# Kernel tuning notes

Measured on AMD Instinct MI355X. Metric: run time of the kernel, lower is better.

Reference implementation:

```python
import jax, jax.numpy as jnp
import numpy as np
from jax import lax

V, E, H = 32000, 256, 512
B, S_SRC, S_TGT = 32, 128, 64


def setup_inputs() -> dict:
    key = jax.random.key(0)
    ks = jax.random.split(key, 16)
    n = lambda k, shp: jax.random.normal(k, shp, dtype=jnp.float32) * 0.05
    return {
        "src": jax.random.randint(ks[0], (B, S_SRC), 0, V, dtype=jnp.int32),
        "tgt": jax.random.randint(ks[1], (B, S_TGT), 0, V, dtype=jnp.int32),
        "enc_emb": n(ks[2], (V, E)),
        "enc_Wih": n(ks[3], (4 * H, E)),
        "enc_Whh": n(ks[4], (4 * H, H)),
        "enc_b": n(ks[5], (4 * H,)),
        "attn_W": n(ks[6], (H, 2 * H)),
        "attn_b": n(ks[7], (H,)),
        "attn_v": jax.random.uniform(ks[8], (H,), dtype=jnp.float32),
        "dec_emb": n(ks[9], (V, E)),
        "dec_Wih": n(ks[10], (4 * H, E + H)),
        "dec_Whh": n(ks[11], (4 * H, H)),
        "dec_b": n(ks[12], (4 * H,)),
        "out_W": n(ks[13], (V, H)),
        "out_b": n(ks[14], (V,)),
    }


def _lstm_cell(x, h, c, Wih, Whh, b):
    # PyTorch gate order: i, f, g, o. b = b_ih + b_hh fused.
    z = x @ Wih.T + h @ Whh.T + b  # [B, 4H]
    i, f, g, o = jnp.split(z, 4, axis=-1)
    c_new = jax.nn.sigmoid(f) * c + jax.nn.sigmoid(i) * jnp.tanh(g)
    h_new = jax.nn.sigmoid(o) * jnp.tanh(c_new)
    return h_new, c_new


def reference(src, tgt, enc_emb, enc_Wih, enc_Whh, enc_b, attn_W, attn_b,
              attn_v, dec_emb, dec_Wih, dec_Whh, dec_b, out_W, out_b):
    b = src.shape[0]
    h0 = jnp.zeros((b, H), dtype=enc_emb.dtype)
    c0 = jnp.zeros((b, H), dtype=enc_emb.dtype)

    # ---- Encoder: single-layer LSTM over src ----
    emb_src = enc_emb[src]  # [B, S_src, E]

    def enc_step(carry, x_t):
        h, c = carry
        h, c = _lstm_cell(x_t, h, c, enc_Wih, enc_Whh, enc_b)
        return (h, c), h

    (h, c), enc_out = lax.scan(enc_step, (h0, c0), emb_src.transpose(1, 0, 2))
    enc_out = enc_out.transpose(1, 0, 2)  # [B, S_src, H]

    # attn_W acts on cat([hidden, enc]); split into hidden and encoder parts.
    W_h = attn_W[:, :H]   # [H, H]
    W_e = attn_W[:, H:]   # [H, H]
    enc_proj = jnp.einsum('bsh,kh->bsk', enc_out, W_e)  # precomputed [B, S, H]

    # ---- Decoder with per-step Bahdanau attention ----
    emb_tgt = dec_emb[tgt].transpose(1, 0, 2)  # [T, B, E]

    def dec_step(carry, e_t):
        h, c = carry
        energy = jnp.tanh(enc_proj + (h @ W_h.T + attn_b)[:, None, :])  # [B,S,H]
        score = energy @ attn_v                                          # [B,S]
        a = jax.nn.softmax(score, axis=1)
        context = jnp.einsum('bs,bsh->bh', a, enc_out)                   # [B,H]
        x = jnp.concatenate([e_t, context], axis=-1)                     # [B,E+H]
        h, c = _lstm_cell(x, h, c, dec_Wih, dec_Whh, dec_b)
        return (h, c), h

    _, dec_h = lax.scan(dec_step, (h, c), emb_tgt)
    dec_h = dec_h.transpose(1, 0, 2)  # [B, T, H]

    return dec_h @ out_W.T + out_b  # [B, T, V]
```

## Files before the change

kernel.cpp:

```cpp
#include <hip/hip_runtime.h>

#define B_    32
#define SSRC  128
#define STGT  64
#define E_    256
#define H_    512
#define G4    2048
#define V_    32000

typedef unsigned short u16;
typedef short bf16x8 __attribute__((ext_vector_type(8)));
typedef float f32x4 __attribute__((ext_vector_type(4)));

__device__ __forceinline__ u16 f2b(float f) {
  unsigned u = __float_as_uint(f);
  u += 0x7FFFu + ((u >> 16) & 1u);
  return (u16)(u >> 16);
}
__device__ __forceinline__ float b2f(u16 h) {
  return __uint_as_float(((unsigned)h) << 16);
}
__device__ __forceinline__ unsigned pk2(float lo, float hi) {
  return (unsigned)f2b(lo) | (((unsigned)f2b(hi)) << 16);
}
__device__ __forceinline__ float sigm(float x) { return 1.0f / (1.0f + __expf(-x)); }
__device__ __forceinline__ float tanh_(float x) { return 1.0f - 2.0f / (1.0f + __expf(2.0f * x)); }

#if defined(__has_builtin)
#if __has_builtin(__builtin_amdgcn_fdot2_f32_bf16)
#define HAS_DOT2 1
#endif
#endif
#ifdef HAS_DOT2
typedef __bf16 b162 __attribute__((ext_vector_type(2)));
__device__ __forceinline__ float dot2u(unsigned a, unsigned b, float acc) {
  return __builtin_amdgcn_fdot2_f32_bf16(__builtin_bit_cast(b162, a),
                                         __builtin_bit_cast(b162, b), acc, false);
}
#else
__device__ __forceinline__ float dot2u(unsigned a, unsigned b, float acc) {
  acc += __uint_as_float(a << 16) * __uint_as_float(b << 16);
  acc += __uint_as_float(a & 0xffff0000u) * __uint_as_float(b & 0xffff0000u);
  return acc;
}
#endif
__device__ __forceinline__ float dot4(uint4 w, uint4 h, float acc) {
  return dot2u(w.w, h.w, dot2u(w.z, h.z, dot2u(w.y, h.y, dot2u(w.x, h.x, acc))));
}

__device__ __forceinline__ int swz64(int c) {
  return (c & ~3) | ((c & 3) ^ ((c >> 3) & 3));
}

__device__ __forceinline__ uint4 cload4(const void* p) {
  uint4 r;
  asm volatile("global_load_dwordx4 %0, %1, off sc0 sc1\n\ts_waitcnt vmcnt(0)"
               : "=&v"(r) : "v"(p) : "memory");
  return r;
}
__device__ __forceinline__ void cload4x2(uint4& a, uint4& b, const void* pa, const void* pb) {
  asm volatile("global_load_dwordx4 %0, %2, off sc0 sc1\n\t"
               "global_load_dwordx4 %1, %3, off sc0 sc1\n\t"
               "s_waitcnt vmcnt(0)"
               : "=&v"(a), "=&v"(b) : "v"(pa), "v"(pb) : "memory");
}
__device__ __forceinline__ void cstoreu(unsigned* p, unsigned v) {
  asm volatile("global_store_dword %0, %1, off sc0 sc1" :: "v"(p), "v"(v) : "memory");
}
__device__ __forceinline__ void cstore4(unsigned* p, uint4 v) {
  cstoreu(p + 0, v.x);
  cstoreu(p + 1, v.y);
  cstoreu(p + 2, v.z);
  cstoreu(p + 3, v.w);
}

__device__ __forceinline__ void gbar(int* flags, int myid, int target) {
  asm volatile("s_waitcnt vmcnt(0)" ::: "memory");
  __syncthreads();
  if (threadIdx.x == 0)
    __hip_atomic_store(flags + myid, target, __ATOMIC_RELAXED, __HIP_MEMORY_SCOPE_AGENT);
  if (threadIdx.x < 64) {
    int l = threadIdx.x & 31;
    while (__hip_atomic_load(flags + l, __ATOMIC_RELAXED, __HIP_MEMORY_SCOPE_AGENT) < target)
      __builtin_amdgcn_s_sleep(1);
  }
  __syncthreads();
  asm volatile("" ::: "memory");
}

__global__ void prep_kernel(const int* __restrict__ src, const int* __restrict__ tgt,
                            const float* __restrict__ enc_emb, const float* __restrict__ dec_emb,
                            const float* __restrict__ enc_Wih, const float* __restrict__ dec_Wih,
                            const float* __restrict__ attn_W, const float* __restrict__ out_W,
                            u16* __restrict__ A_enc, u16* __restrict__ A_dec,
                            u16* __restrict__ WihE, u16* __restrict__ WihD,
                            u16* __restrict__ Web, u16* __restrict__ WihCp,
                            u16* __restrict__ outWb)
{
  const long n_outw = (long)V_ * H_;
  const long n_aenc = (long)B_ * SSRC * E_;
  const long n_adec = (long)B_ * STGT * E_;
  const long n_wih  = (long)G4 * E_;
  const long n_web  = (long)H_ * H_;
  const long n_wcp  = (long)G4 * H_;
  const long total = n_outw + n_aenc + n_adec + 2 * n_wih + n_web + n_wcp;
  for (long i = (long)blockIdx.x * blockDim.x + threadIdx.x; i < total;
       i += (long)gridDim.x * blockDim.x) {
    long x = i;
    if (x < n_outw) { outWb[x] = f2b(out_W[x]); continue; }
    x -= n_outw;
    if (x < n_aenc) {
      int row = (int)(x >> 8), e = (int)(x & 255);
      A_enc[x] = f2b(enc_emb[(size_t)src[row] * E_ + e]);
      continue;
    }
    x -= n_aenc;
    if (x < n_adec) {
      int row = (int)(x >> 8), e = (int)(x & 255);
      A_dec[x] = f2b(dec_emb[(size_t)tgt[row] * E_ + e]);
      continue;
    }
    x -= n_adec;
    if (x < n_wih) { WihE[x] = f2b(enc_Wih[x]); continue; }
    x -= n_wih;
    if (x < n_wih) {
      int r = (int)(x >> 8), e = (int)(x & 255);
      WihD[x] = f2b(dec_Wih[(size_t)r * 768 + e]);
      continue;
    }
    x -= n_wih;
    if (x < n_web) {
      int d = (int)(x >> 9), k = (int)(x & 511);
      Web[x] = f2b(attn_W[(size_t)d * 1024 + 512 + k]);
      continue;
    }
    x -= n_web;
    {
      int n = (int)(x >> 9), k = (int)(x & 511);
      int gb = n >> 6, gate = (n >> 4) & 3, jl = n & 15;
      int orig = gate * 512 + gb * 16 + jl;
      WihCp[x] = f2b(dec_Wih[(size_t)orig * 768 + 256 + k]);
    }
  }
}

template<int KTOT, bool OBF>
__global__ __launch_bounds__(256, 2) void gemm_nt(
    const u16* __restrict__ A, const u16* __restrict__ Bm,
    const float* __restrict__ bias, void* __restrict__ Cv, int M, int N)
{
  int nbm = M >> 7;
  int bn = blockIdx.x / nbm;
  int bm = blockIdx.x % nbm;
  int w = threadIdx.x >> 6, l = threadIdx.x & 63;
  int wr = w >> 1, wc = w & 1;
  int m0 = bm * 128 + wr * 64, n0 = bn * 128 + wc * 64;
  int lr = l & 15, ko = (l >> 4) * 8;
  f32x4 acc[4][4] = {};
  const u16* Ap = A + (size_t)(m0 + lr) * KTOT + ko;
  const u16* Bp = Bm + (size_t)(n0 + lr) * KTOT + ko;
  for (int k0 = 0; k0 < KTOT; k0 += 32) {
    bf16x8 af[4], bfr[4];
#pragma unroll
    for (int i = 0; i < 4; ++i) af[i] = *(const bf16x8*)(Ap + (size_t)i * 16 * KTOT + k0);
#pragma unroll
    for (int i = 0; i < 4; ++i) bfr[i] = *(const bf16x8*)(Bp + (size_t)i * 16 * KTOT + k0);
#pragma unroll
    for (int i = 0; i < 4; ++i)
#pragma unroll
      for (int j = 0; j < 4; ++j)
        acc[i][j] = __builtin_amdgcn_mfma_f32_16x16x32_bf16(af[i], bfr[j], acc[i][j], 0, 0, 0);
  }
  int rbase = (l >> 4) * 4;
#pragma unroll
  for (int i = 0; i < 4; ++i) {
#pragma unroll
    for (int j = 0; j < 4; ++j) {
      int gn = n0 + j * 16 + lr;
      float bv = bias ? bias[gn] : 0.f;
#pragma unroll
      for (int r = 0; r < 4; ++r) {
        int gm = m0 + i * 16 + rbase + r;
        float v = acc[i][j][r] + bv;
        if (OBF) ((u16*)Cv)[(size_t)gm * N + gn] = f2b(v);
        else     ((float*)Cv)[(size_t)gm * N + gn] = v;
      }
    }
  }
}

__device__ __forceinline__ void zgemv64(int tid, const uint4* Wu, const uint4* Hu,
                                        float (*part)[64][4]) {
  int rq = tid >> 4, kq = tid & 15;
  float acc[4][4] = {};
#pragma unroll
  for (int u = 0; u < 4; ++u) {
    int sc = swz64(kq * 4 + u);
    uint4 h0 = Hu[sc], h1 = Hu[64 + sc], h2 = Hu[128 + sc], h3 = Hu[192 + sc];
#pragma unroll
    for (int r = 0; r < 4; ++r) {
      uint4 wv = Wu[(rq * 4 + r) * 64 + sc];
      acc[r][0] = dot4(wv, h0, acc[r][0]);
      acc[r][1] = dot4(wv, h1, acc[r][1]);
      acc[r][2] = dot4(wv, h2, acc[r][2]);
      acc[r][3] = dot4(wv, h3, acc[r][3]);
    }
  }
#pragma unroll
  for (int r = 0; r < 4; ++r) {
    float4 v = {acc[r][0], acc[r][1], acc[r][2], acc[r][3]};
    *(float4*)&part[kq][(rq * 4 + r) ^ (kq & 7)][0] = v;
  }
}

template<typename GrowF>
__device__ __forceinline__ void fillw64(int tid, const float* Wsrc, uint4* Wu, GrowF grow) {
#pragma unroll 4
  for (int i = 0; i < 16; ++i) {
    int idx4 = tid + i * 256;
    int row = idx4 >> 6, c = idx4 & 63;
    const float* s = Wsrc + (size_t)grow(row) * 512 + c * 8;
    float4 a = *(const float4*)s, b4 = *(const float4*)(s + 4);
    uint4 pkv = {pk2(a.x, a.y), pk2(a.z, a.w), pk2(b4.x, b4.y), pk2(b4.z, b4.w)};
    Wu[row * 64 + swz64(c)] = pkv;
  }
}

__global__ __launch_bounds__(256, 1) void encoder_kernel(
    const float* __restrict__ enc_Whh, const u16* __restrict__ encXW,
    unsigned* __restrict__ h16buf ,
    float* __restrict__ cfin, u16* __restrict__ eo_g, int* __restrict__ bars)
{
  const int tid = threadIdx.x;
  const int g = blockIdx.x & 7;
  const int gb = blockIdx.x >> 3;
  const int b0 = g * 4;
  const int ds0 = gb * 16;
  int* flags = bars + g * 64;
  int ep_ = 0;

  __shared__ uint4 encW4[64 * 64];
  __shared__ uint4 hl16[4 * 64];
  __shared__ float part[16][64][4];
  __shared__ float zx[4][64];
  __shared__ float cS[4][16];

  if (tid < 64) cS[tid >> 4][tid & 15] = 0.f;
  fillw64(tid, enc_Whh, encW4, [&](int row) { return (row >> 4) * 512 + ds0 + (row & 15); });
  __syncthreads();

  for (int t = 0; t < SSRC; ++t) {
    {
      int row = tid >> 6, c = tid & 63;
      uint4 v = cload4((const uint4*)h16buf + (size_t)(t & 1) * 2048 + (b0 + row) * 64 + c);
      hl16[row * 64 + swz64(c)] = v;
    }
    __syncthreads();
    zgemv64(tid, encW4, hl16, part);
    __syncthreads();
    {
      int b_l = tid >> 6, rl = tid & 63;
      float z = 0.f;
#pragma unroll
      for (int kq = 0; kq < 16; ++kq) z += part[kq][rl ^ (kq & 7)][b_l];
      int grow = (rl >> 4) * 512 + ds0 + (rl & 15);
      z += b2f(encXW[((size_t)(b0 + b_l) * SSRC + t) * G4 + grow]);
      zx[b_l][rl] = z;
    }
    __syncthreads();
    if (tid < 64) {
      int bl = tid >> 4, jl = tid & 15;
      float iv = zx[bl][jl], fv = zx[bl][16 + jl], gv = zx[bl][32 + jl], ov = zx[bl][48 + jl];
      float cn = sigm(fv) * cS[bl][jl] + sigm(iv) * tanh_(gv);
      float hn = sigm(ov) * tanh_(cn);
      cS[bl][jl] = cn;
      eo_g[((size_t)(b0 + bl) * SSRC + t) * H_ + ds0 + jl] = f2b(hn);
      float hn1 = __shfl_down(hn, 1);
      if ((jl & 1) == 0)
        cstoreu(h16buf + (size_t)((t + 1) & 1) * 8192 + (size_t)(b0 + bl) * 256 + gb * 8 + (jl >> 1),
                pk2(hn, hn1));
    }
    gbar(flags, gb, ++ep_);
  }
  if (tid < 64)
    cfin[(size_t)(b0 + (tid >> 4)) * H_ + ds0 + (tid & 15)] = cS[tid >> 4][tid & 15];
}

__global__ __launch_bounds__(256, 1) void decoder_kernel(
    const float* __restrict__ dec_Whh, const float* __restrict__ attn_W,
    const float* __restrict__ attn_b, const float* __restrict__ attn_v,
    const u16* __restrict__ eprojb, const u16* __restrict__ decXW,
    const u16* __restrict__ eoPb,
    unsigned* __restrict__ hd16 , const float* __restrict__ cfin,
    float* __restrict__ qg , float* __restrict__ scoreb ,
    u16* __restrict__ dech, int* __restrict__ bars)
{
  const int tid = threadIdx.x;
  const int g = blockIdx.x & 7;
  const int gb = blockIdx.x >> 3;
  const int b0 = g * 4;
  const int ds0 = gb * 16;
  int* flags = bars + g * 64;
  int ep_ = 0;

  __shared__ uint4 decW4[64 * 64];
  __shared__ uint4 Whb4[16 * 64];
  __shared__ uint4 hl16[4 * 64];
  __shared__ float part[16][64][4];
  __shared__ float partE[8][64][4];
  __shared__ float4 qf4[4 * 128];
  __shared__ float4 vf4[128];
  __shared__ float scoreS[4][128];
  __shared__ float aS[4][128];
  __shared__ float zx[4][64];
  __shared__ __align__(16) float qS[4][16];
  __shared__ __align__(16) float scr16[4][4];
  __shared__ float cS[4][16];
  __shared__ float bS[16];

  if (tid < 64) cS[tid >> 4][tid & 15] = cfin[(size_t)(b0 + (tid >> 4)) * H_ + ds0 + (tid & 15)];
  if (tid < 16) bS[tid] = attn_b[ds0 + tid];
  if (tid < 128) {
    float4 v = *(const float4*)(attn_v + tid * 4);
    vf4[tid ^ ((tid >> 3) & 7)] = v;
  }
  fillw64(tid, dec_Whh, decW4, [&](int row) { return (row >> 4) * 512 + ds0 + (row & 15); });
#pragma unroll
  for (int i = 0; i < 4; ++i) {
    int idx4 = tid + i * 256;
    int row = idx4 >> 6, c = idx4 & 63;
    const float* s = attn_W + (size_t)(ds0 + row) * 1024 + c * 8;
    float4 a = *(const float4*)s, b4 = *(const float4*)(s + 4);
    uint4 pkv = {pk2(a.x, a.y), pk2(a.z, a.w), pk2(b4.x, b4.y), pk2(b4.z, b4.w)};
    Whb4[row * 64 + (c ^ (row & 7))] = pkv;
  }
  __syncthreads();

  for (int t = 0; t < STGT; ++t) {
    {
      int row = tid >> 6, c = tid & 63;
      uint4 v = cload4((const uint4*)hd16 + (b0 + row) * 64 + c);
      hl16[row * 64 + swz64(c)] = v;
    }
    __syncthreads();
    {
      int b_l = tid >> 6, d_l = (tid >> 2) & 15, kq4 = tid & 3;
      float acc = 0.f;
#pragma unroll
      for (int u = 0; u < 16; ++u) {
        int c = kq4 * 16 + u;
        uint4 wv = Whb4[d_l * 64 + (c ^ (d_l & 7))];
        uint4 hv = hl16[b_l * 64 + swz64(c)];
        acc = dot4(wv, hv, acc);
      }
      acc += __shfl_xor(acc, 1);
      acc += __shfl_xor(acc, 2);
      if (kq4 == 0) qS[b_l][d_l] = acc + bS[d_l];
    }
    __syncthreads();
    if (tid < 16) {
      float4 v = *(float4*)&qS[tid >> 2][(tid & 3) * 4];
      cstore4((unsigned*)(qg + (size_t)(g * 4 + (tid >> 2)) * 512 + ds0 + (tid & 3) * 4),
              *(uint4*)&v);
    }
    gbar(flags, gb, ++ep_);

    {
      int b_l = tid >> 6, c = tid & 63;
      uint4 a, b4;
      const float* sp = qg + (size_t)(g * 4 + b_l) * 512 + c * 8;
      cload4x2(a, b4, sp, sp + 4);
      int lw0 = c * 2, lw1 = c * 2 + 1;
      qf4[b_l * 128 + (lw0 ^ ((lw0 >> 3) & 7))] = *(float4*)&a;
      qf4[b_l * 128 + (lw1 ^ ((lw1 >> 3) & 7))] = *(float4*)&b4;
    }
    __syncthreads();
    {
      int p = tid >> 4, lane16 = tid & 15;
      int b_l = p >> 2, s_l = p & 3;
      int s = gb * 4 + s_l;
      const uint4* ep = (const uint4*)(eprojb + ((size_t)(b0 + b_l) * SSRC + s) * H_) + lane16 * 4;
      uint4 e0 = ep[0], e1 = ep[1], e2 = ep[2], e3 = ep[3];
      unsigned ev[8] = {e0.x, e0.y, e0.z, e0.w, e1.x, e1.y, e1.z, e1.w};
      unsigned ev2[8] = {e2.x, e2.y, e2.z, e2.w, e3.x, e3.y, e3.z, e3.w};
      float acc = 0.f;
#pragma unroll
      for (int i = 0; i < 8; ++i) {
        int lr = lane16 * 8 + i;
        float4 q = qf4[b_l * 128 + (lr ^ ((lr >> 3) & 7))];
        float4 vv = vf4[lr ^ ((lr >> 3) & 7)];
        unsigned lo = (i < 4) ? ev[i * 2] : ev2[(i - 4) * 2];
        unsigned hi = (i < 4) ? ev[i * 2 + 1] : ev2[(i - 4) * 2 + 1];
        acc += vv.x * tanh_(b2f((u16)(lo & 0xffff)) + q.x);
        acc += vv.y * tanh_(b2f((u16)(lo >> 16)) + q.y);
        acc += vv.z * tanh_(b2f((u16)(hi & 0xffff)) + q.z);
        acc += vv.w * tanh_(b2f((u16)(hi >> 16)) + q.w);
      }
      acc += __shfl_xor(acc, 1);
      acc += __shfl_xor(acc, 2);
      acc += __shfl_xor(acc, 4);
      acc += __shfl_xor(acc, 8);
      if (lane16 == 0) scr16[b_l][s_l] = acc;
    }
    __syncthreads();
    if (tid < 4) {
      float4 v = *(float4*)&scr16[tid][0];
      cstore4((unsigned*)(scoreb + (size_t)(g * 4 + tid) * 128 + gb * 4), *(uint4*)&v);
    }
    gbar(flags, gb, ++ep_);

    if (tid < 128) {
      int row = tid >> 5, c4 = tid & 31;
      uint4 vv = cload4(scoreb + (size_t)(g * 4 + row) * 128 + c4 * 4);
      *(float4*)&scoreS[row][c4 * 4] = *(float4*)&vv;
    }
    zgemv64(tid, decW4, hl16, part);
    __syncthreads();
    {
      int w = tid >> 6, lane = tid & 63;
      float s1 = scoreS[w][lane], s2v = scoreS[w][64 + lane];
      float m = fmaxf(s1, s2v);
#pragma unroll
      for (int off = 32; off; off >>= 1) m = fmaxf(m, __shfl_xor(m, off));
      float e1 = __expf(s1 - m), e2 = __expf(s2v - m);
      float sm = e1 + e2;
#pragma unroll
      for (int off = 32; off; off >>= 1) sm += __shfl_xor(sm, off);
      float inv = 1.0f / sm;
      aS[w][lane] = e1 * inv;
      aS[w][64 + lane] = e2 * inv;
    }
    __syncthreads();
    {
      int sq = tid >> 5, cp = tid & 31;
      const unsigned* eoPu = (const unsigned*)eoPb;
      float a0 = 0.f, a1 = 0.f, a2 = 0.f, a3 = 0.f, a4 = 0.f, a5 = 0.f, a6 = 0.f, a7 = 0.f;
#pragma unroll 4
      for (int s = sq * 16; s < sq * 16 + 16; ++s) {
        unsigned u0 = eoPu[((size_t)(b0 + 0) * SSRC + s) * 1024 + gb * 32 + cp];
        unsigned u1 = eoPu[((size_t)(b0 + 1) * SSRC + s) * 1024 + gb * 32 + cp];
        unsigned u2 = eoPu[((size_t)(b0 + 2) * SSRC + s) * 1024 + gb * 32 + cp];
        unsigned u3 = eoPu[((size_t)(b0 + 3) * SSRC + s) * 1024 + gb * 32 + cp];
        float w0 = aS[0][s], w1 = aS[1][s], w2 = aS[2][s], w3 = aS[3][s];
        a0 += w0 * b2f((u16)(u0 & 0xffff)); a1 += w0 * b2f((u16)(u0 >> 16));
        a2 += w1 * b2f((u16)(u1 & 0xffff)); a3 += w1 * b2f((u16)(u1 >> 16));
        a4 += w2 * b2f((u16)(u2 & 0xffff)); a5 += w2 * b2f((u16)(u2 >> 16));
        a6 += w3 * b2f((u16)(u3 & 0xffff)); a7 += w3 * b2f((u16)(u3 >> 16));
      }
      float4 lo = {a0, a2, a4, a6}, hi = {a1, a3, a5, a7};
      *(float4*)&partE[sq][cp * 2][0] = lo;
      *(float4*)&partE[sq][cp * 2 + 1][0] = hi;
    }
    __syncthreads();
    {
      int b_l = tid >> 6, rl = tid & 63;
      float z = 0.f;
#pragma unroll
      for (int kq = 0; kq < 16; ++kq) z += part[kq][rl ^ (kq & 7)][b_l];
#pragma unroll
      for (int sq = 0; sq < 8; ++sq) z += partE[sq][rl][b_l];
      int grow = (rl >> 4) * 512 + ds0 + (rl & 15);
      z += b2f(decXW[((size_t)(b0 + b_l) * STGT + t) * G4 + grow]);
      zx[b_l][rl] = z;
    }
    __syncthreads();
    if (tid < 64) {
      int bl = tid >> 4, jl = tid & 15;
      float iv = zx[bl][jl], fv = zx[bl][16 + jl], gv = zx[bl][32 + jl], ov = zx[bl][48 + jl];
      float cn = sigm(fv) * cS[bl][jl] + sigm(iv) * tanh_(gv);
      float hn = sigm(ov) * tanh_(cn);
      cS[bl][jl] = cn;
      dech[((size_t)(b0 + bl) * STGT + t) * H_ + ds0 + jl] = f2b(hn);
      float hn1 = __shfl_down(hn, 1);
      if ((jl & 1) == 0)
        cstoreu(hd16 + (size_t)(b0 + bl) * 256 + gb * 8 + (jl >> 1), pk2(hn, hn1));
    }
    gbar(flags, gb, ++ep_);
  }
}

#define OFF_BARE   0u
#define OFF_BARD   2048u
#define OFF_H16    4096u
#define OFF_CFIN   69632u
#define OFF_QG     135168u
#define OFF_SCORE  200704u
#define OFF_AENC   262144u
#define OFF_ADEC   2359296u
#define OFF_WIHE   3407872u
#define OFF_WIHD   4456448u
#define OFF_WEB    5505024u
#define OFF_WIHCP  6029312u
#define OFF_OUTW   8126464u
#define OFF_ENCXW  40894464u
#define OFF_DECXW  57671680u
#define OFF_EO     66060288u
#define OFF_EPROJ  70254592u
#define OFF_DECH   74448896u

extern "C" void kernel_launch(void* const* d_in, const int* in_sizes, int n_in,
                              void* d_out, int out_size, void* d_ws, size_t ws_size,
                              hipStream_t stream)
{
  const int*   src     = (const int*)d_in[0];
  const int*   tgt     = (const int*)d_in[1];
  const float* enc_emb = (const float*)d_in[2];
  const float* enc_Wih = (const float*)d_in[3];
  const float* enc_Whh = (const float*)d_in[4];
  const float* enc_b   = (const float*)d_in[5];
  const float* attn_W  = (const float*)d_in[6];
  const float* attn_b  = (const float*)d_in[7];
  const float* attn_v  = (const float*)d_in[8];
  const float* dec_emb = (const float*)d_in[9];
  const float* dec_Wih = (const float*)d_in[10];
  const float* dec_Whh = (const float*)d_in[11];
  const float* dec_b   = (const float*)d_in[12];
  const float* out_W   = (const float*)d_in[13];
  const float* out_b   = (const float*)d_in[14];

  char* ws = (char*)d_ws;
  int*      barE   = (int*)(ws + OFF_BARE);
  int*      barD   = (int*)(ws + OFF_BARD);
  unsigned* h16buf = (unsigned*)(ws + OFF_H16);
  float*    cfin   = (float*)(ws + OFF_CFIN);
  float*    qg     = (float*)(ws + OFF_QG);
  float*    scoreb = (float*)(ws + OFF_SCORE);
  u16*      A_enc  = (u16*)(ws + OFF_AENC);
  u16*      A_dec  = (u16*)(ws + OFF_ADEC);
  u16*      WihE   = (u16*)(ws + OFF_WIHE);
  u16*      WihD   = (u16*)(ws + OFF_WIHD);
  u16*      Web    = (u16*)(ws + OFF_WEB);
  u16*      WihCp  = (u16*)(ws + OFF_WIHCP);
  u16*      outWb  = (u16*)(ws + OFF_OUTW);
  u16*      encXW  = (u16*)(ws + OFF_ENCXW);
  u16*      eoPb   = (u16*)(ws + OFF_ENCXW);
  u16*      decXW  = (u16*)(ws + OFF_DECXW);
  u16*      eo_g   = (u16*)(ws + OFF_EO);
  u16*      eprojb = (u16*)(ws + OFF_EPROJ);
  u16*      dech   = (u16*)(ws + OFF_DECH);

  (void)hipMemsetAsync(d_ws, 0, OFF_H16 + 65536, stream);

  prep_kernel<<<2048, 256, 0, stream>>>(src, tgt, enc_emb, dec_emb, enc_Wih, dec_Wih,
                                        attn_W, out_W, A_enc, A_dec, WihE, WihD, Web, WihCp, outWb);

  gemm_nt<256, true><<<512, 256, 0, stream>>>(A_enc, WihE, enc_b, (void*)encXW, 4096, 2048);
  gemm_nt<256, true><<<256, 256, 0, stream>>>(A_dec, WihD, dec_b, (void*)decXW, 2048, 2048);

  encoder_kernel<<<256, 256, 0, stream>>>(enc_Whh, encXW, h16buf, cfin, eo_g, barE);

  gemm_nt<512, true><<<128, 256, 0, stream>>>(eo_g, Web, nullptr, (void*)eprojb, 4096, 512);
  gemm_nt<512, true><<<512, 256, 0, stream>>>(eo_g, WihCp, nullptr, (void*)eoPb, 4096, 2048);

  decoder_kernel<<<256, 256, 0, stream>>>(dec_Whh, attn_W, attn_b, attn_v,
                                          eprojb, decXW, eoPb, h16buf, cfin,
                                          qg, scoreb, dech, barD);

  gemm_nt<512, false><<<4000, 256, 0, stream>>>(dech, outWb, out_b, d_out, 2048, 32000);
}
```

Baseline: 1.555 ms.

## Fuse encoder projections into recurrent loop and cut decoder attention barriers

The encoder kernel now computes the attention encoder projection and the context-times-Wih projection for the previous step's hidden state inside its barrier wait window, which removes two separate GEMM launches and the eo_g intermediate. The decoder replaces the global query exchange plus score exchange (two barriers) with per-block partial scores over each block's own 16 hidden dimensions, written to a buffer and reduced after a single split arrive/wait barrier that overlaps the Whh GEMV. Encoder-output projections are also preloaded into registers once per block. The cost is extra serial work per encoder step, many small scattered global stores, and a 32-way cross-block reduction of partial scores on every decoder step.

```diff
diff --git a/kernel.cpp b/kernel.cpp
--- a/kernel.cpp
+++ b/kernel.cpp
@@ -9,6 +9,7 @@
 #define V_    32000
 
 typedef unsigned short u16;
+typedef unsigned long long u64b;
 typedef short bf16x8 __attribute__((ext_vector_type(8)));
 typedef float f32x4 __attribute__((ext_vector_type(4)));
 
@@ -58,27 +59,23 @@
                : "=&v"(r) : "v"(p) : "memory");
   return r;
 }
-__device__ __forceinline__ void cload4x2(uint4& a, uint4& b, const void* pa, const void* pb) {
-  asm volatile("global_load_dwordx4 %0, %2, off sc0 sc1\n\t"
-               "global_load_dwordx4 %1, %3, off sc0 sc1\n\t"
-               "s_waitcnt vmcnt(0)"
-               : "=&v"(a), "=&v"(b) : "v"(pa), "v"(pb) : "memory");
+__device__ __forceinline__ void cstoref(float* p, float v) {
+  asm volatile("global_store_dword %0, %1, off sc0 sc1" :: "v"(p), "v"(v) : "memory");
 }
 __device__ __forceinline__ void cstoreu(unsigned* p, unsigned v) {
   asm volatile("global_store_dword %0, %1, off sc0 sc1" :: "v"(p), "v"(v) : "memory");
 }
-__device__ __forceinline__ void cstore4(unsigned* p, uint4 v) {
-  cstoreu(p + 0, v.x);
-  cstoreu(p + 1, v.y);
-  cstoreu(p + 2, v.z);
-  cstoreu(p + 3, v.w);
-}
-
-__device__ __forceinline__ void gbar(int* flags, int myid, int target) {
+__device__ __forceinline__ float cloadf_relaxed(const float* p) {
+  return __hip_atomic_load(p, __ATOMIC_RELAXED, __HIP_MEMORY_SCOPE_AGENT);
+}
+
+__device__ __forceinline__ void arrive(int* flags, int myid, int target) {
   asm volatile("s_waitcnt vmcnt(0)" ::: "memory");
   __syncthreads();
   if (threadIdx.x == 0)
     __hip_atomic_store(flags + myid, target, __ATOMIC_RELAXED, __HIP_MEMORY_SCOPE_AGENT);
+}
+__device__ __forceinline__ void waitbar(int* flags, int target) {
   if (threadIdx.x < 64) {
     int l = threadIdx.x & 31;
     while (__hip_atomic_load(flags + l, __ATOMIC_RELAXED, __HIP_MEMORY_SCOPE_AGENT) < target)
@@ -91,19 +88,17 @@
 __global__ void prep_kernel(const int* __restrict__ src, const int* __restrict__ tgt,
                             const float* __restrict__ enc_emb, const float* __restrict__ dec_emb,
                             const float* __restrict__ enc_Wih, const float* __restrict__ dec_Wih,
-                            const float* __restrict__ attn_W, const float* __restrict__ out_W,
+                            const float* __restrict__ out_W,
                             u16* __restrict__ A_enc, u16* __restrict__ A_dec,
                             u16* __restrict__ WihE, u16* __restrict__ WihD,
-                            u16* __restrict__ Web, u16* __restrict__ WihCp,
-                            u16* __restrict__ outWb)
+                            u16* __restrict__ WihC, u16* __restrict__ outWb)
 {
   const long n_outw = (long)V_ * H_;
   const long n_aenc = (long)B_ * SSRC * E_;
   const long n_adec = (long)B_ * STGT * E_;
   const long n_wih  = (long)G4 * E_;
-  const long n_web  = (long)H_ * H_;
   const long n_wcp  = (long)G4 * H_;
-  const long total = n_outw + n_aenc + n_adec + 2 * n_wih + n_web + n_wcp;
+  const long total = n_outw + n_aenc + n_adec + 2 * n_wih + n_wcp;
   for (long i = (long)blockIdx.x * blockDim.x + threadIdx.x; i < total;
        i += (long)gridDim.x * blockDim.x) {
     long x = i;
@@ -129,17 +124,9 @@
       continue;
     }
     x -= n_wih;
-    if (x < n_web) {
-      int d = (int)(x >> 9), k = (int)(x & 511);
-      Web[x] = f2b(attn_W[(size_t)d * 1024 + 512 + k]);
-      continue;
-    }
-    x -= n_web;
-    {
-      int n = (int)(x >> 9), k = (int)(x & 511);
-      int gb = n >> 6, gate = (n >> 4) & 3, jl = n & 15;
-      int orig = gate * 512 + gb * 16 + jl;
-      WihCp[x] = f2b(dec_Wih[(size_t)orig * 768 + 256 + k]);
+    {
+      int r = (int)(x >> 9), k = (int)(x & 511);
+      WihC[x] = f2b(dec_Wih[(size_t)r * 768 + 256 + k]);
     }
   }
 }
@@ -177,7 +164,7 @@
 #pragma unroll
     for (int j = 0; j < 4; ++j) {
       int gn = n0 + j * 16 + lr;
-      float bv = bias ? bias[gn] : 0.f;
+      float bv = bias[gn];
 #pragma unroll
       for (int r = 0; r < 4; ++r) {
         int gm = m0 + i * 16 + rbase + r;
@@ -227,9 +214,10 @@
 }
 
 __global__ __launch_bounds__(256, 1) void encoder_kernel(
-    const float* __restrict__ enc_Whh, const u16* __restrict__ encXW,
-    unsigned* __restrict__ h16buf ,
-    float* __restrict__ cfin, u16* __restrict__ eo_g, int* __restrict__ bars)
+    const float* __restrict__ enc_Whh, const float* __restrict__ attn_W,
+    const u16* __restrict__ WihC, const u16* __restrict__ encXW,
+    unsigned* __restrict__ h16buf, float* __restrict__ cfin,
+    u16* __restrict__ eprojb, u16* __restrict__ eoPw, int* __restrict__ bars)
 {
   const int tid = threadIdx.x;
   const int g = blockIdx.x & 7;
@@ -237,9 +225,9 @@
   const int b0 = g * 4;
   const int ds0 = gb * 16;
   int* flags = bars + g * 64;
-  int ep_ = 0;
 
   __shared__ uint4 encW4[64 * 64];
+  __shared__ uint4 web4[16 * 64];
   __shared__ uint4 hl16[4 * 64];
   __shared__ float part[16][64][4];
   __shared__ float zx[4][64];
@@ -247,6 +235,15 @@
 
   if (tid < 64) cS[tid >> 4][tid & 15] = 0.f;
   fillw64(tid, enc_Whh, encW4, [&](int row) { return (row >> 4) * 512 + ds0 + (row & 15); });
+#pragma unroll
+  for (int i = 0; i < 4; ++i) {
+    int idx4 = tid + i * 256;
+    int row = idx4 >> 6, c = idx4 & 63;
+    const float* s = attn_W + (size_t)(ds0 + row) * 1024 + 512 + c * 8;
+    float4 a = *(const float4*)s, b4 = *(const float4*)(s + 4);
+    uint4 pkv = {pk2(a.x, a.y), pk2(a.z, a.w), pk2(b4.x, b4.y), pk2(b4.z, b4.w)};
+    web4[row * 64 + (c ^ (row & 7))] = pkv;
+  }
   __syncthreads();
 
   for (int t = 0; t < SSRC; ++t) {
@@ -274,13 +271,103 @@
       float cn = sigm(fv) * cS[bl][jl] + sigm(iv) * tanh_(gv);
       float hn = sigm(ov) * tanh_(cn);
       cS[bl][jl] = cn;
-      eo_g[((size_t)(b0 + bl) * SSRC + t) * H_ + ds0 + jl] = f2b(hn);
       float hn1 = __shfl_down(hn, 1);
       if ((jl & 1) == 0)
         cstoreu(h16buf + (size_t)((t + 1) & 1) * 8192 + (size_t)(b0 + bl) * 256 + gb * 8 + (jl >> 1),
                 pk2(hn, hn1));
     }
-    gbar(flags, gb, ++ep_);
+    arrive(flags, gb, t + 1);
+    if (t > 0) {
+      int tm1 = t - 1;
+      {
+        int d_l = tid >> 4, b_l = (tid >> 2) & 3, kq4 = tid & 3;
+        float acc = 0.f;
+#pragma unroll
+        for (int u = 0; u < 16; ++u) {
+          int c = kq4 * 16 + u;
+          acc = dot4(web4[d_l * 64 + (c ^ (d_l & 7))], hl16[b_l * 64 + swz64(c)], acc);
+        }
+        acc += __shfl_xor(acc, 1);
+        acc += __shfl_xor(acc, 2);
+        if (kq4 == 0)
+          eprojb[(((size_t)(b0 + b_l) * SSRC + tm1) << 9) + ds0 + d_l] = f2b(acc);
+      }
+      {
+        int r = tid >> 2, kq4 = tid & 3;
+        int n = (r >> 4) * 512 + ds0 + (r & 15);
+        const uint4* wr_ = (const uint4*)(WihC + (size_t)n * 512) + kq4 * 16;
+        float a0 = 0.f, a1 = 0.f, a2 = 0.f, a3 = 0.f;
+#pragma unroll
+        for (int u = 0; u < 16; ++u) {
+          uint4 wv = wr_[u];
+          int sc = swz64(kq4 * 16 + u);
+          a0 = dot4(wv, hl16[sc], a0);
+          a1 = dot4(wv, hl16[64 + sc], a1);
+          a2 = dot4(wv, hl16[128 + sc], a2);
+          a3 = dot4(wv, hl16[192 + sc], a3);
+        }
+        a0 += __shfl_xor(a0, 1); a0 += __shfl_xor(a0, 2);
+        a1 += __shfl_xor(a1, 1); a1 += __shfl_xor(a1, 2);
+        a2 += __shfl_xor(a2, 1); a2 += __shfl_xor(a2, 2);
+        a3 += __shfl_xor(a3, 1); a3 += __shfl_xor(a3, 2);
+        if (kq4 == 0) {
+          size_t base = ((size_t)b0 * SSRC + tm1) << 11;
+          eoPw[base + n] = f2b(a0);
+          eoPw[base + (SSRC << 11) + n] = f2b(a1);
+          eoPw[base + (2u * SSRC << 11) + n] = f2b(a2);
+          eoPw[base + (3u * SSRC << 11) + n] = f2b(a3);
+        }
+      }
+    }
+    waitbar(flags, t + 1);
+  }
+  {
+    int row = tid >> 6, c = tid & 63;
+    uint4 v = cload4((const uint4*)h16buf + (b0 + row) * 64 + c);
+    hl16[row * 64 + swz64(c)] = v;
+  }
+  __syncthreads();
+  {
+    int tm1 = SSRC - 1;
+    {
+      int d_l = tid >> 4, b_l = (tid >> 2) & 3, kq4 = tid & 3;
+      float acc = 0.f;
+#pragma unroll
+      for (int u = 0; u < 16; ++u) {
+        int c = kq4 * 16 + u;
+        acc = dot4(web4[d_l * 64 + (c ^ (d_l & 7))], hl16[b_l * 64 + swz64(c)], acc);
+      }
+      acc += __shfl_xor(acc, 1);
+      acc += __shfl_xor(acc, 2);
+      if (kq4 == 0)
+        eprojb[(((size_t)(b0 + b_l) * SSRC + tm1) << 9) + ds0 + d_l] = f2b(acc);
+    }
+    {
+      int r = tid >> 2, kq4 = tid & 3;
+      int n = (r >> 4) * 512 + ds0 + (r & 15);
+      const uint4* wr_ = (const uint4*)(WihC + (size_t)n * 512) + kq4 * 16;
+      float a0 = 0.f, a1 = 0.f, a2 = 0.f, a3 = 0.f;
+#pragma unroll
+      for (int u = 0; u < 16; ++u) {
+        uint4 wv = wr_[u];
+        int sc = swz64(kq4 * 16 + u);
+        a0 = dot4(wv, hl16[sc], a0);
+        a1 = dot4(wv, hl16[64 + sc], a1);
+        a2 = dot4(wv, hl16[128 + sc], a2);
+        a3 = dot4(wv, hl16[192 + sc], a3);
+      }
+      a0 += __shfl_xor(a0, 1); a0 += __shfl_xor(a0, 2);
+      a1 += __shfl_xor(a1, 1); a1 += __shfl_xor(a1, 2);
+      a2 += __shfl_xor(a2, 1); a2 += __shfl_xor(a2, 2);
+      a3 += __shfl_xor(a3, 1); a3 += __shfl_xor(a3, 2);
+      if (kq4 == 0) {
+        size_t base = ((size_t)b0 * SSRC + tm1) << 11;
+        eoPw[base + n] = f2b(a0);
+        eoPw[base + (SSRC << 11) + n] = f2b(a1);
+        eoPw[base + (2u * SSRC << 11) + n] = f2b(a2);
+        eoPw[base + (3u * SSRC << 11) + n] = f2b(a3);
+      }
+    }
   }
   if (tid < 64)
     cfin[(size_t)(b0 + (tid >> 4)) * H_ + ds0 + (tid & 15)] = cS[tid >> 4][tid & 15];
@@ -291,8 +378,8 @@
     const float* __restrict__ attn_b, const float* __restrict__ attn_v,
     const u16* __restrict__ eprojb, const u16* __restrict__ decXW,
     const u16* __restrict__ eoPb,
-    unsigned* __restrict__ hd16 , const float* __restrict__ cfin,
-    float* __restrict__ qg , float* __restrict__ scoreb ,
+    unsigned* __restrict__ hd16, const float* __restrict__ cfin,
+    float* __restrict__ vpart ,
     u16* __restrict__ dech, int* __restrict__ bars)
 {
   const int tid = threadIdx.x;
@@ -308,22 +395,15 @@
   __shared__ uint4 hl16[4 * 64];
   __shared__ float part[16][64][4];
   __shared__ float partE[8][64][4];
-  __shared__ float4 qf4[4 * 128];
-  __shared__ float4 vf4[128];
   __shared__ float scoreS[4][128];
   __shared__ float aS[4][128];
   __shared__ float zx[4][64];
-  __shared__ __align__(16) float qS[4][16];
-  __shared__ __align__(16) float scr16[4][4];
+  __shared__ float qS[4][16];
   __shared__ float cS[4][16];
-  __shared__ float bS[16];
+  __shared__ float vS[16], bS[16];
 
   if (tid < 64) cS[tid >> 4][tid & 15] = cfin[(size_t)(b0 + (tid >> 4)) * H_ + ds0 + (tid & 15)];
-  if (tid < 16) bS[tid] = attn_b[ds0 + tid];
-  if (tid < 128) {
-    float4 v = *(const float4*)(attn_v + tid * 4);
-    vf4[tid ^ ((tid >> 3) & 7)] = v;
-  }
+  if (tid < 16) { vS[tid] = attn_v[ds0 + tid]; bS[tid] = attn_b[ds0 + tid]; }
   fillw64(tid, dec_Whh, decW4, [&](int row) { return (row >> 4) * 512 + ds0 + (row & 15); });
 #pragma unroll
   for (int i = 0; i < 4; ++i) {
@@ -334,6 +414,20 @@
     uint4 pkv = {pk2(a.x, a.y), pk2(a.z, a.w), pk2(b4.x, b4.y), pk2(b4.z, b4.w)};
     Whb4[row * 64 + (c ^ (row & 7))] = pkv;
   }
+  const int sq = tid >> 5, cp = tid & 31;
+  const int n32 = (cp >> 3) * 256 + gb * 8 + (cp & 7);
+  uint4 eor[16];
+  {
+    const unsigned* eoPu = (const unsigned*)eoPb;
+#pragma unroll
+    for (int si = 0; si < 16; ++si) {
+      int s = sq * 16 + si;
+      eor[si].x = eoPu[((size_t)(b0 + 0) * SSRC + s) * 1024 + n32];
+      eor[si].y = eoPu[((size_t)(b0 + 1) * SSRC + s) * 1024 + n32];
+      eor[si].z = eoPu[((size_t)(b0 + 2) * SSRC + s) * 1024 + n32];
+      eor[si].w = eoPu[((size_t)(b0 + 3) * SSRC + s) * 1024 + n32];
+    }
+  }
   __syncthreads();
 
   for (int t = 0; t < STGT; ++t) {
@@ -349,72 +443,57 @@
 #pragma unroll
       for (int u = 0; u < 16; ++u) {
         int c = kq4 * 16 + u;
-        uint4 wv = Whb4[d_l * 64 + (c ^ (d_l & 7))];
-        uint4 hv = hl16[b_l * 64 + swz64(c)];
-        acc = dot4(wv, hv, acc);
+        acc = dot4(Whb4[d_l * 64 + (c ^ (d_l & 7))], hl16[b_l * 64 + swz64(c)], acc);
       }
       acc += __shfl_xor(acc, 1);
       acc += __shfl_xor(acc, 2);
       if (kq4 == 0) qS[b_l][d_l] = acc + bS[d_l];
     }
     __syncthreads();
-    if (tid < 16) {
-      float4 v = *(float4*)&qS[tid >> 2][(tid & 3) * 4];
-      cstore4((unsigned*)(qg + (size_t)(g * 4 + (tid >> 2)) * 512 + ds0 + (tid & 3) * 4),
-              *(uint4*)&v);
-    }
-    gbar(flags, gb, ++ep_);
-
-    {
-      int b_l = tid >> 6, c = tid & 63;
-      uint4 a, b4;
-      const float* sp = qg + (size_t)(g * 4 + b_l) * 512 + c * 8;
-      cload4x2(a, b4, sp, sp + 4);
-      int lw0 = c * 2, lw1 = c * 2 + 1;
-      qf4[b_l * 128 + (lw0 ^ ((lw0 >> 3) & 7))] = *(float4*)&a;
-      qf4[b_l * 128 + (lw1 ^ ((lw1 >> 3) & 7))] = *(float4*)&b4;
-    }
-    __syncthreads();
-    {
-      int p = tid >> 4, lane16 = tid & 15;
-      int b_l = p >> 2, s_l = p & 3;
-      int s = gb * 4 + s_l;
-      const uint4* ep = (const uint4*)(eprojb + ((size_t)(b0 + b_l) * SSRC + s) * H_) + lane16 * 4;
-      uint4 e0 = ep[0], e1 = ep[1], e2 = ep[2], e3 = ep[3];
-      unsigned ev[8] = {e0.x, e0.y, e0.z, e0.w, e1.x, e1.y, e1.z, e1.w};
-      unsigned ev2[8] = {e2.x, e2.y, e2.z, e2.w, e3.x, e3.y, e3.z, e3.w};
-      float acc = 0.f;
-#pragma unroll
-      for (int i = 0; i < 8; ++i) {
-        int lr = lane16 * 8 + i;
-        float4 q = qf4[b_l * 128 + (lr ^ ((lr >> 3) & 7))];
-        float4 vv = vf4[lr ^ ((lr >> 3) & 7)];
-        unsigned lo = (i < 4) ? ev[i * 2] : ev2[(i - 4) * 2];
-        unsigned hi = (i < 4) ? ev[i * 2 + 1] : ev2[(i - 4) * 2 + 1];
-        acc += vv.x * tanh_(b2f((u16)(lo & 0xffff)) + q.x);
-        acc += vv.y * tanh_(b2f((u16)(lo >> 16)) + q.y);
-        acc += vv.z * tanh_(b2f((u16)(hi & 0xffff)) + q.z);
-        acc += vv.w * tanh_(b2f((u16)(hi >> 16)) + q.w);
-      }
-      acc += __shfl_xor(acc, 1);
-      acc += __shfl_xor(acc, 2);
-      acc += __shfl_xor(acc, 4);
-      acc += __shfl_xor(acc, 8);
-      if (lane16 == 0) scr16[b_l][s_l] = acc;
-    }
-    __syncthreads();
-    if (tid < 4) {
-      float4 v = *(float4*)&scr16[tid][0];
-      cstore4((unsigned*)(scoreb + (size_t)(g * 4 + tid) * 128 + gb * 4), *(uint4*)&v);
-    }
-    gbar(flags, gb, ++ep_);
-
-    if (tid < 128) {
-      int row = tid >> 5, c4 = tid & 31;
-      uint4 vv = cload4(scoreb + (size_t)(g * 4 + row) * 128 + c4 * 4);
-      *(float4*)&scoreS[row][c4 * 4] = *(float4*)&vv;
-    }
+    {
+      float* vp = vpart + ((size_t)g * 32 + gb) * 512;
+#pragma unroll
+      for (int r = 0; r < 2; ++r) {
+        int idx = tid + r * 256;
+        int b_l = idx >> 7, s = idx & 127;
+        const uint4* ep = (const uint4*)(eprojb + (((size_t)(b0 + b_l) * SSRC + s) << 9) + ds0);
+        uint4 e0 = ep[0], e1 = ep[1];
+        float acc = 0.f;
+        acc += vS[0]  * tanh_(b2f((u16)(e0.x & 0xffff)) + qS[b_l][0]);
+        acc += vS[1]  * tanh_(b2f((u16)(e0.x >> 16))    + qS[b_l][1]);
+        acc += vS[2]  * tanh_(b2f((u16)(e0.y & 0xffff)) + qS[b_l][2]);
+        acc += vS[3]  * tanh_(b2f((u16)(e0.y >> 16))    + qS[b_l][3]);
+        acc += vS[4]  * tanh_(b2f((u16)(e0.z & 0xffff)) + qS[b_l][4]);
+        acc += vS[5]  * tanh_(b2f((u16)(e0.z >> 16))    + qS[b_l][5]);
+        acc += vS[6]  * tanh_(b2f((u16)(e0.w & 0xffff)) + qS[b_l][6]);
+        acc += vS[7]  * tanh_(b2f((u16)(e0.w >> 16))    + qS[b_l][7]);
+        acc += vS[8]  * tanh_(b2f((u16)(e1.x & 0xffff)) + qS[b_l][8]);
+        acc += vS[9]  * tanh_(b2f((u16)(e1.x >> 16))    + qS[b_l][9]);
+        acc += vS[10] * tanh_(b2f((u16)(e1.y & 0xffff)) + qS[b_l][10]);
+        acc += vS[11] * tanh_(b2f((u16)(e1.y >> 16))    + qS[b_l][11]);
+        acc += vS[12] * tanh_(b2f((u16)(e1.z & 0xffff)) + qS[b_l][12]);
+        acc += vS[13] * tanh_(b2f((u16)(e1.z >> 16))    + qS[b_l][13]);
+        acc += vS[14] * tanh_(b2f((u16)(e1.w & 0xffff)) + qS[b_l][14]);
+        acc += vS[15] * tanh_(b2f((u16)(e1.w >> 16))    + qS[b_l][15]);
+        cstoref(vp + idx, acc);
+      }
+    }
+    arrive(flags, gb, ++ep_);
     zgemv64(tid, decW4, hl16, part);
+    waitbar(flags, ep_);
+
+    {
+      int b_l = tid >> 6, s0 = (tid & 63) * 2;
+      float a0 = 0.f, a1 = 0.f;
+#pragma unroll 8
+      for (int j = 0; j < 32; ++j) {
+        const float* p = vpart + ((size_t)g * 32 + j) * 512 + b_l * 128 + s0;
+        a0 += cloadf_relaxed(p);
+        a1 += cloadf_relaxed(p + 1);
+      }
+      scoreS[b_l][s0] = a0;
+      scoreS[b_l][s0 + 1] = a1;
+    }
     __syncthreads();
     {
       int w = tid >> 6, lane = tid & 63;
@@ -432,24 +511,21 @@
     }
     __syncthreads();
     {
-      int sq = tid >> 5, cp = tid & 31;
-      const unsigned* eoPu = (const unsigned*)eoPb;
       float a0 = 0.f, a1 = 0.f, a2 = 0.f, a3 = 0.f, a4 = 0.f, a5 = 0.f, a6 = 0.f, a7 = 0.f;
-#pragma unroll 4
-      for (int s = sq * 16; s < sq * 16 + 16; ++s) {
-        unsigned u0 = eoPu[((size_t)(b0 + 0) * SSRC + s) * 1024 + gb * 32 + cp];
-        unsigned u1 = eoPu[((size_t)(b0 + 1) * SSRC + s) * 1024 + gb * 32 + cp];
-        unsigned u2 = eoPu[((size_t)(b0 + 2) * SSRC + s) * 1024 + gb * 32 + cp];
-        unsigned u3 = eoPu[((size_t)(b0 + 3) * SSRC + s) * 1024 + gb * 32 + cp];
+#pragma unroll
+      for (int si = 0; si < 16; ++si) {
+        int s = sq * 16 + si;
         float w0 = aS[0][s], w1 = aS[1][s], w2 = aS[2][s], w3 = aS[3][s];
+        unsigned u0 = eor[si].x, u1 = eor[si].y, u2 = eor[si].z, u3 = eor[si].w;
         a0 += w0 * b2f((u16)(u0 & 0xffff)); a1 += w0 * b2f((u16)(u0 >> 16));
         a2 += w1 * b2f((u16)(u1 & 0xffff)); a3 += w1 * b2f((u16)(u1 >> 16));
         a4 += w2 * b2f((u16)(u2 & 0xffff)); a5 += w2 * b2f((u16)(u2 >> 16));
         a6 += w3 * b2f((u16)(u3 & 0xffff)); a7 += w3 * b2f((u16)(u3 >> 16));
       }
+      int r0 = (cp >> 3) * 16 + (cp & 7) * 2;
       float4 lo = {a0, a2, a4, a6}, hi = {a1, a3, a5, a7};
-      *(float4*)&partE[sq][cp * 2][0] = lo;
-      *(float4*)&partE[sq][cp * 2 + 1][0] = hi;
+      *(float4*)&partE[sq][r0][0] = lo;
+      *(float4*)&partE[sq][r0 + 1][0] = hi;
     }
     __syncthreads();
     {
@@ -458,7 +534,7 @@
 #pragma unroll
       for (int kq = 0; kq < 16; ++kq) z += part[kq][rl ^ (kq & 7)][b_l];
 #pragma unroll
-      for (int sq = 0; sq < 8; ++sq) z += partE[sq][rl][b_l];
+      for (int sq2 = 0; sq2 < 8; ++sq2) z += partE[sq2][rl][b_l];
       int grow = (rl >> 4) * 512 + ds0 + (rl & 15);
       z += b2f(decXW[((size_t)(b0 + b_l) * STGT + t) * G4 + grow]);
       zx[b_l][rl] = z;
@@ -475,7 +551,8 @@
       if ((jl & 1) == 0)
         cstoreu(hd16 + (size_t)(b0 + bl) * 256 + gb * 8 + (jl >> 1), pk2(hn, hn1));
     }
-    gbar(flags, gb, ++ep_);
+    arrive(flags, gb, ++ep_);
+    waitbar(flags, ep_);
   }
 }
 
@@ -483,20 +560,17 @@
 #define OFF_BARD   2048u
 #define OFF_H16    4096u
 #define OFF_CFIN   69632u
-#define OFF_QG     135168u
-#define OFF_SCORE  200704u
-#define OFF_AENC   262144u
-#define OFF_ADEC   2359296u
-#define OFF_WIHE   3407872u
-#define OFF_WIHD   4456448u
-#define OFF_WEB    5505024u
-#define OFF_WIHCP  6029312u
-#define OFF_OUTW   8126464u
-#define OFF_ENCXW  40894464u
-#define OFF_DECXW  57671680u
-#define OFF_EO     66060288u
-#define OFF_EPROJ  70254592u
-#define OFF_DECH   74448896u
+#define OFF_VPART  135168u
+#define OFF_AENC   1048576u
+#define OFF_ADEC   3145728u
+#define OFF_WIHE   4194304u
+#define OFF_WIHD   5242880u
+#define OFF_WIHC   6291456u
+#define OFF_OUTW   8388608u
+#define OFF_ENCXW  41943040u
+#define OFF_DECXW  58720256u
+#define OFF_EPROJ  67108864u
+#define OFF_DECH   71303168u
 
 extern "C" void kernel_launch(void* const* d_in, const int* in_sizes, int n_in,
                               void* d_out, int out_size, void* d_ws, size_t ws_size,
@@ -523,38 +597,33 @@
   int*      barD   = (int*)(ws + OFF_BARD);
   unsigned* h16buf = (unsigned*)(ws + OFF_H16);
   float*    cfin   = (float*)(ws + OFF_CFIN);
-  float*    qg     = (float*)(ws + OFF_QG);
-  float*    scoreb = (float*)(ws + OFF_SCORE);
+  float*    vpart  = (float*)(ws + OFF_VPART);
   u16*      A_enc  = (u16*)(ws + OFF_AENC);
   u16*      A_dec  = (u16*)(ws + OFF_ADEC);
   u16*      WihE   = (u16*)(ws + OFF_WIHE);
   u16*      WihD   = (u16*)(ws + OFF_WIHD);
-  u16*      Web    = (u16*)(ws + OFF_WEB);
-  u16*      WihCp  = (u16*)(ws + OFF_WIHCP);
+  u16*      WihC   = (u16*)(ws + OFF_WIHC);
   u16*      outWb  = (u16*)(ws + OFF_OUTW);
   u16*      encXW  = (u16*)(ws + OFF_ENCXW);
   u16*      eoPb   = (u16*)(ws + OFF_ENCXW);
   u16*      decXW  = (u16*)(ws + OFF_DECXW);
-  u16*      eo_g   = (u16*)(ws + OFF_EO);
   u16*      eprojb = (u16*)(ws + OFF_EPROJ);
   u16*      dech   = (u16*)(ws + OFF_DECH);
 
   (void)hipMemsetAsync(d_ws, 0, OFF_H16 + 65536, stream);
 
   prep_kernel<<<2048, 256, 0, stream>>>(src, tgt, enc_emb, dec_emb, enc_Wih, dec_Wih,
-                                        attn_W, out_W, A_enc, A_dec, WihE, WihD, Web, WihCp, outWb);
+                                        out_W, A_enc, A_dec, WihE, WihD, WihC, outWb);
 
   gemm_nt<256, true><<<512, 256, 0, stream>>>(A_enc, WihE, enc_b, (void*)encXW, 4096, 2048);
   gemm_nt<256, true><<<256, 256, 0, stream>>>(A_dec, WihD, dec_b, (void*)decXW, 2048, 2048);
 
-  encoder_kernel<<<256, 256, 0, stream>>>(enc_Whh, encXW, h16buf, cfin, eo_g, barE);
-
-  gemm_nt<512, true><<<128, 256, 0, stream>>>(eo_g, Web, nullptr, (void*)eprojb, 4096, 512);
-  gemm_nt<512, true><<<512, 256, 0, stream>>>(eo_g, WihCp, nullptr, (void*)eoPb, 4096, 2048);
+  encoder_kernel<<<256, 256, 0, stream>>>(enc_Whh, attn_W, WihC, encXW,
+                                          h16buf, cfin, eprojb, eoPb, barE);
 
   decoder_kernel<<<256, 256, 0, stream>>>(dec_Whh, attn_W, attn_b, attn_v,
                                           eprojb, decXW, eoPb, h16buf, cfin,
-                                          qg, scoreb, dech, barD);
+                                          vpart, dech, barD);
 
   gemm_nt<512, false><<<4000, 256, 0, stream>>>(dech, outWb, out_b, d_out, 2048, 32000);
 }
```

New measurement: 1.735 ms. 1.12x slower.
